# Optimization experiments

Measured on AMD Instinct MI355X. Metric: run time of the kernel, lower is better.

The kernel has to match this reference:

```python
import jax, jax.numpy as jnp
from jax import lax
import numpy as np

INPUT_SIZE = 8
HIDDEN = 32
OUTPUT = 1
B, T = 8192, 512


def setup_inputs() -> dict:
    key = jax.random.key(0)
    ks = jax.random.split(key, 8)
    s = 1.0 / np.sqrt(HIDDEN)  # PyTorch LSTM init scale
    x = jax.random.normal(ks[0], (B, T, INPUT_SIZE), dtype=jnp.float32)
    W_ih = jax.random.uniform(ks[1], (4 * HIDDEN, INPUT_SIZE), minval=-s, maxval=s, dtype=jnp.float32)
    W_hh = jax.random.uniform(ks[2], (4 * HIDDEN, HIDDEN), minval=-s, maxval=s, dtype=jnp.float32)
    b_ih = jax.random.uniform(ks[3], (4 * HIDDEN,), minval=-s, maxval=s, dtype=jnp.float32)
    b_hh = jax.random.uniform(ks[4], (4 * HIDDEN,), minval=-s, maxval=s, dtype=jnp.float32)
    W_fc = jax.random.uniform(ks[5], (OUTPUT, HIDDEN), minval=-s, maxval=s, dtype=jnp.float32)
    b_fc = jax.random.uniform(ks[6], (OUTPUT,), minval=-s, maxval=s, dtype=jnp.float32)
    return {"x": x, "W_ih": W_ih, "W_hh": W_hh, "b_ih": b_ih, "b_hh": b_hh, "W_fc": W_fc, "b_fc": b_fc}


def reference(x, W_ih, W_hh, b_ih, b_hh, W_fc, b_fc):
    # x: [B, T, D]. Precompute input-gate contributions in one large GEMM,
    # then scan the recurrence over time. PyTorch gate order: i, f, g, o.
    Bn, Tn, _ = x.shape
    H = W_hh.shape[1]
    xg = jnp.einsum('btd,gd->btg', x, W_ih) + b_ih + b_hh  # [B, T, 4H]
    xg = jnp.swapaxes(xg, 0, 1)  # [T, B, 4H]

    def step(carry, xt):
        h, c = carry
        gates = xt + h @ W_hh.T  # [B, 4H]
        i, f, g, o = jnp.split(gates, 4, axis=-1)
        c = jax.nn.sigmoid(f) * c + jax.nn.sigmoid(i) * jnp.tanh(g)
        h = jax.nn.sigmoid(o) * jnp.tanh(c)
        return (h, c), None

    h0 = jnp.zeros((Bn, H), dtype=x.dtype)
    (h_n, _), _ = lax.scan(step, (h0, h0), xg)
    # fc applied to h_n: [num_layers=1, B, H] -> [1, B, output_size]
    out = h_n @ W_fc.T + b_fc  # [B, 1]
    return out[None, :, :]
```

## Files before the change

kernel.cpp:

```cpp
#include <hip/hip_runtime.h>
#include <cstddef>

#define T_LEN 512
#define IN_D 8
#define H 32
#define NBATCH 16
#define NT 512
#define NCHUNK (T_LEN / 8)
#define LOG2E 1.44269504088896341f
#define GP 36
#define CSCLAMP 88.f

typedef __attribute__((ext_vector_type(8))) short bf16x8;
typedef __attribute__((ext_vector_type(4))) float f32x4;

__device__ __forceinline__ float fexp2(float v) { return __builtin_amdgcn_exp2f(v); }
__device__ __forceinline__ float frcp(float v)  { return __builtin_amdgcn_rcpf(v); }
__device__ __forceinline__ unsigned short f2bf(float f) {
    unsigned u = __builtin_bit_cast(unsigned, f);
    u += 0x7FFF + ((u >> 16) & 1);
    return (unsigned short)(u >> 16);
}
__device__ __forceinline__ float bf2f(unsigned short b) {
    unsigned u = ((unsigned)b) << 16;
    return __builtin_bit_cast(float, u);
}
__device__ __forceinline__ float ubits(unsigned u) { return __builtin_bit_cast(float, u); }
__device__ __forceinline__ unsigned cvt_pk_bf16(float lo, float hi) {
    unsigned r;
    asm("v_cvt_pk_bf16_f32 %0, %1, %2" : "=v"(r) : "v"(lo), "v"(hi));
    return r;
}

#define WG_BARRIER() asm volatile("s_waitcnt lgkmcnt(0)\n\ts_barrier" ::: "memory")

__global__ void __launch_bounds__(NT, 4) lstm_mfma4(
    const float* __restrict__ x, const float* __restrict__ W_ih,
    const float* __restrict__ W_hh, const float* __restrict__ b_ih,
    const float* __restrict__ b_hh, const float* __restrict__ W_fc,
    const float* __restrict__ b_fc, float* __restrict__ out)
{
    __shared__ __align__(16) float G[4][NBATCH][GP];
    __shared__ __align__(16) unsigned short hhi[NBATCH][48];
    __shared__ __align__(16) unsigned short hlo[NBATCH][48];
    __shared__ __align__(16) unsigned short xstg[8][17][24];

    const int tix  = threadIdx.x;
    const int w    = tix >> 6;
    const int g    = w >> 1;
    const int d    = w & 1;
    const int lane = tix & 63;
    const int q    = lane >> 4;
    const int cc   = lane & 15;

    const float kk = (g == 2) ? -2.f * LOG2E : -LOG2E;

    bf16x8 Bh, Bl, Bx;
    const int r = 16 * (2 * g + d) + cc;
    #pragma unroll
    for (int j = 0; j < 8; ++j) {
        const int p = 8 * q + j;
        const int u = 16 * (p & 1) + (p >> 1);
        const float ws = kk * W_hh[r * H + u];
        const unsigned short whi = f2bf(ws);
        Bh[j] = (short)whi;
        Bl[j] = (short)f2bf(ws - bf2f(whi));
        if (q == 3) {
            Bx[j] = 0;
        } else {
            const float wsx = kk * W_ih[r * IN_D + j];
            const unsigned short xwh = f2bf(wsx);
            Bx[j] = (q == 2) ? (short)f2bf(wsx - bf2f(xwh)) : (short)xwh;
        }
    }
    const float bias = kk * (b_ih[r] + b_hh[r]);
    const f32x4 biasv = { bias, bias, bias, bias };

    const int xoff = (q == 2) ? 0 : ((q == 3) ? 16 : 8 * q);

    const int xb = (tix >> 4) & 15, xs = (tix >> 1) & 7, xhf = tix & 1;
    const bool stager = (tix < 256);
    const float* xbase = x + (size_t)(blockIdx.x * NBATCH + xb) * (size_t)(T_LEN * IN_D)
                           + xs * IN_D + 4 * xhf;
    auto ldchunk = [&](int ch) { return *(const float4*)(xbase + (size_t)ch * 8 * IN_D); };
    auto stage = [&](float4 v) {
        const unsigned h0 = cvt_pk_bf16(v.x, v.y);
        const unsigned h1 = cvt_pk_bf16(v.z, v.w);
        const unsigned l0 = cvt_pk_bf16(v.x - ubits(h0 << 16), v.y - ubits(h0 & 0xffff0000u));
        const unsigned l1 = cvt_pk_bf16(v.z - ubits(h1 << 16), v.w - ubits(h1 & 0xffff0000u));
        *(uint2*)&xstg[xs][xb][4 * xhf]     = make_uint2(h0, h1);
        *(uint2*)&xstg[xs][xb][8 + 4 * xhf] = make_uint2(l0, l1);
    };

    for (int i = tix; i < NBATCH * 48 / 2; i += NT) {
        ((unsigned*)hhi)[i] = 0u;
        ((unsigned*)hlo)[i] = 0u;
    }
    for (int i = tix; i < 8 * 17 * 24 / 2; i += NT) ((unsigned*)xstg)[i] = 0u;
    __syncthreads();
    float4 xbuf = {0.f, 0.f, 0.f, 0.f};
    if (stager) {
        stage(ldchunk(0));
        xbuf = ldchunk(1);
    }
    __syncthreads();

    f32x4 XC[8];
#define REFILL(j) do { \
        const bf16x8 Ax_ = *(const bf16x8*)&xstg[(j)][cc][xoff]; \
        XC[(j)] = __builtin_amdgcn_mfma_f32_16x16x32_bf16(Ax_, Bx, biasv, 0, 0, 0); \
    } while (0)
    #pragma unroll
    for (int s = 0; s < 8; ++s) REFILL(s);

    const int m = tix >> 5, u = tix & 31;
    const float wfc = W_fc[u];
    const float TWL = 2.f * LOG2E;
    float cs = 0.f, hf = 0.f;

    for (int blk = 0; blk < NCHUNK; ++blk) {
        #pragma unroll
        for (int s = 0; s < 8; ++s) {
            const bf16x8 A0 = *(const bf16x8*)&hhi[cc][8 * q];
            const bf16x8 A2 = *(const bf16x8*)&hlo[cc][8 * q];
            const f32x4 z = { 0.f, 0.f, 0.f, 0.f };
            f32x4 a1 = __builtin_amdgcn_mfma_f32_16x16x32_bf16(A0, Bh, XC[s], 0, 0, 0);
            f32x4 a2 = __builtin_amdgcn_mfma_f32_16x16x32_bf16(A2, Bh, z, 0, 0, 0);
            a2 = __builtin_amdgcn_mfma_f32_16x16x32_bf16(A0, Bl, a2, 0, 0, 0);
            const f32x4 C = a1 + a2;

            if (s == 0 && stager) {
                stage(xbuf);
                int nc = blk + 2;
                if (nc > NCHUNK - 1) nc = NCHUNK - 1;
                xbuf = ldchunk(nc);
            }

            #pragma unroll
            for (int rg = 0; rg < 4; ++rg)
                G[g][4 * q + rg][cc + 16 * d] = C[rg];

            if (s >= 1) REFILL(s - 1);
            if (s == 7) REFILL(7);

            WG_BARRIER();

            {
                const float Ei = fexp2(G[0][m][u]);
                const float Ef = fexp2(G[1][m][u]);
                const float Eg = fexp2(G[2][m][u]);
                const float Eo = fexp2(G[3][m][u]);
                const float P  = (1.f + Eg) * (1.f + Ei);
                const float Q  = 1.f + Ef;
                const float r1 = __builtin_fmaf(Eg, -TWL, TWL);
                const float num = __builtin_fmaf(cs, P, r1 * Q);
                const float rd  = frcp(P * Q);
                cs = num * rd;
                cs = fminf(fmaxf(cs, -CSCLAMP), CSCLAMP);
                const float W  = fexp2(cs);
                const float rh = frcp((1.f + Eo) * (W + 1.f));
                hf = (W - 1.f) * rh;
                const float hp = __shfl_xor(hf, 16);
                if ((tix & 16) == 0) {
                    const unsigned hw = cvt_pk_bf16(hf, hp);
                    const unsigned lw = cvt_pk_bf16(hf - ubits(hw << 16),
                                                    hp - ubits(hw & 0xffff0000u));
                    *(unsigned*)&hhi[m][2 * (u & 15)] = hw;
                    *(unsigned*)&hlo[m][2 * (u & 15)] = lw;
                }
            }

            WG_BARRIER();
        }
    }
#undef REFILL

    float sacc = hf * wfc;
    sacc += __shfl_xor(sacc, 1);
    sacc += __shfl_xor(sacc, 2);
    sacc += __shfl_xor(sacc, 4);
    sacc += __shfl_xor(sacc, 8);
    sacc += __shfl_xor(sacc, 16);
    if ((tix & 31) == 0) out[blockIdx.x * NBATCH + m] = sacc + b_fc[0];
}

extern "C" void kernel_launch(void* const* d_in, const int* in_sizes, int n_in,
                              void* d_out, int out_size, void* d_ws, size_t ws_size,
                              hipStream_t stream) {
    const float* x    = (const float*)d_in[0];
    const float* W_ih = (const float*)d_in[1];
    const float* W_hh = (const float*)d_in[2];
    const float* b_ih = (const float*)d_in[3];
    const float* b_hh = (const float*)d_in[4];
    const float* W_fc = (const float*)d_in[5];
    const float* b_fc = (const float*)d_in[6];
    float* out = (float*)d_out;
    const int Bn = in_sizes[0] / (T_LEN * IN_D);
    lstm_mfma4<<<dim3(Bn / NBATCH), dim3(NT), 0, stream>>>(
        x, W_ih, W_hh, b_ih, b_hh, W_fc, b_fc, out);
}
```

Measured before the change: 473.8 us.

## Interleave gate rows so each lane holds all four gates, dropping gate LDS exchange

Reorders the W_hh/W_ih rows so that every MFMA output lane receives the i,f,g,o pre-activations of a single hidden unit and batch row. The gate LDS buffer and one of the two workgroup barriers per timestep can therefore be removed. The hidden state becomes double-buffered so writes for step t+1 do not collide with reads of step t, and the final FC reduction now goes through a small LDS partial-sum array. The cost is more scattered 16-bit LDS stores of h and a third independent MFMA for the low-order correction term.

```diff
diff --git a/kernel.cpp b/kernel.cpp
--- a/kernel.cpp
+++ b/kernel.cpp
@@ -8,7 +8,6 @@
 #define NT 512
 #define NCHUNK (T_LEN / 8)
 #define LOG2E 1.44269504088896341f
-#define GP 36
 #define CSCLAMP 88.f
 
 typedef __attribute__((ext_vector_type(8))) short bf16x8;
@@ -34,47 +33,51 @@
 
 #define WG_BARRIER() asm volatile("s_waitcnt lgkmcnt(0)\n\ts_barrier" ::: "memory")
 
-__global__ void __launch_bounds__(NT, 4) lstm_mfma4(
+__global__ void __launch_bounds__(NT, 4) lstm_xfree(
     const float* __restrict__ x, const float* __restrict__ W_ih,
     const float* __restrict__ W_hh, const float* __restrict__ b_ih,
     const float* __restrict__ b_hh, const float* __restrict__ W_fc,
     const float* __restrict__ b_fc, float* __restrict__ out)
 {
-    __shared__ __align__(16) float G[4][NBATCH][GP];
-    __shared__ __align__(16) unsigned short hhi[NBATCH][48];
-    __shared__ __align__(16) unsigned short hlo[NBATCH][48];
+    __shared__ __align__(16) unsigned short hh[2][NBATCH][40];
+    __shared__ __align__(16) unsigned short hl[2][NBATCH][40];
     __shared__ __align__(16) unsigned short xstg[8][17][24];
+    __shared__ float gpart[8][NBATCH];
 
     const int tix  = threadIdx.x;
-    const int w    = tix >> 6;
-    const int g    = w >> 1;
-    const int d    = w & 1;
+    const int m    = tix >> 6;
     const int lane = tix & 63;
     const int q    = lane >> 4;
     const int cc   = lane & 15;
 
-    const float kk = (g == 2) ? -2.f * LOG2E : -LOG2E;
-
-    bf16x8 Bh, Bl, Bx;
-    const int r = 16 * (2 * g + d) + cc;
+    const int gate = cc & 3;
+    const int urow = 4 * m + (cc >> 2);
+    const int wrow = 32 * gate + urow;
+    const float kk = (gate == 2) ? -2.f * LOG2E : -LOG2E;
+    bf16x8 Whi, Wlo, Wx;
     #pragma unroll
     for (int j = 0; j < 8; ++j) {
         const int p = 8 * q + j;
         const int u = 16 * (p & 1) + (p >> 1);
-        const float ws = kk * W_hh[r * H + u];
+        const float ws = kk * W_hh[wrow * H + u];
         const unsigned short whi = f2bf(ws);
-        Bh[j] = (short)whi;
-        Bl[j] = (short)f2bf(ws - bf2f(whi));
+        Whi[j] = (short)whi;
+        Wlo[j] = (short)f2bf(ws - bf2f(whi));
         if (q == 3) {
-            Bx[j] = 0;
+            Wx[j] = 0;
         } else {
-            const float wsx = kk * W_ih[r * IN_D + j];
+            const float wsx = kk * W_ih[wrow * IN_D + j];
             const unsigned short xwh = f2bf(wsx);
-            Bx[j] = (q == 2) ? (short)f2bf(wsx - bf2f(xwh)) : (short)xwh;
+            Wx[j] = (q == 2) ? (short)f2bf(wsx - bf2f(xwh)) : (short)xwh;
         }
     }
-    const float bias = kk * (b_ih[r] + b_hh[r]);
-    const f32x4 biasv = { bias, bias, bias, bias };
+    f32x4 biasv;
+    #pragma unroll
+    for (int reg = 0; reg < 4; ++reg) {
+        const int br = 32 * reg + 4 * m + q;
+        const float kkr = (reg == 2) ? -2.f * LOG2E : -LOG2E;
+        biasv[reg] = kkr * (b_ih[br] + b_hh[br]);
+    }
 
     const int xoff = (q == 2) ? 0 : ((q == 3) ? 16 : 8 * q);
 
@@ -92,9 +95,9 @@
         *(uint2*)&xstg[xs][xb][8 + 4 * xhf] = make_uint2(l0, l1);
     };
 
-    for (int i = tix; i < NBATCH * 48 / 2; i += NT) {
-        ((unsigned*)hhi)[i] = 0u;
-        ((unsigned*)hlo)[i] = 0u;
+    for (int i = tix; i < (int)(sizeof(hh) / 4); i += NT) {
+        ((unsigned*)hh)[i] = 0u;
+        ((unsigned*)hl)[i] = 0u;
     }
     for (int i = tix; i < 8 * 17 * 24 / 2; i += NT) ((unsigned*)xstg)[i] = 0u;
     __syncthreads();
@@ -106,28 +109,37 @@
     __syncthreads();
 
     f32x4 XC[8];
-#define REFILL(j) do { \
-        const bf16x8 Ax_ = *(const bf16x8*)&xstg[(j)][cc][xoff]; \
-        XC[(j)] = __builtin_amdgcn_mfma_f32_16x16x32_bf16(Ax_, Bx, biasv, 0, 0, 0); \
-    } while (0)
     #pragma unroll
-    for (int s = 0; s < 8; ++s) REFILL(s);
-
-    const int m = tix >> 5, u = tix & 31;
-    const float wfc = W_fc[u];
+    for (int s = 0; s < 8; ++s) {
+        const bf16x8 Bx_ = *(const bf16x8*)&xstg[s][cc][xoff];
+        XC[s] = __builtin_amdgcn_mfma_f32_16x16x32_bf16(Wx, Bx_, biasv, 0, 0, 0);
+    }
+
+    const int uown = 4 * m + q;
+    const int piu  = (uown < 16) ? 2 * uown : 2 * (uown - 16) + 1;
     const float TWL = 2.f * LOG2E;
     float cs = 0.f, hf = 0.f;
 
     for (int blk = 0; blk < NCHUNK; ++blk) {
         #pragma unroll
         for (int s = 0; s < 8; ++s) {
-            const bf16x8 A0 = *(const bf16x8*)&hhi[cc][8 * q];
-            const bf16x8 A2 = *(const bf16x8*)&hlo[cc][8 * q];
+            const int rb = s & 1, wb = rb ^ 1;
+
+            const bf16x8 Hh = *(const bf16x8*)&hh[rb][cc][8 * q];
+            const bf16x8 Hl = *(const bf16x8*)&hl[rb][cc][8 * q];
+            bf16x8 Bxp, Bx7;
+            if (s >= 1)  Bxp = *(const bf16x8*)&xstg[s - 1][cc][xoff];
+            if (s == 7)  Bx7 = *(const bf16x8*)&xstg[7][cc][xoff];
+
             const f32x4 z = { 0.f, 0.f, 0.f, 0.f };
-            f32x4 a1 = __builtin_amdgcn_mfma_f32_16x16x32_bf16(A0, Bh, XC[s], 0, 0, 0);
-            f32x4 a2 = __builtin_amdgcn_mfma_f32_16x16x32_bf16(A2, Bh, z, 0, 0, 0);
-            a2 = __builtin_amdgcn_mfma_f32_16x16x32_bf16(A0, Bl, a2, 0, 0, 0);
-            const f32x4 C = a1 + a2;
+            f32x4 a1 = __builtin_amdgcn_mfma_f32_16x16x32_bf16(Whi, Hh, XC[s], 0, 0, 0);
+            f32x4 a2 = __builtin_amdgcn_mfma_f32_16x16x32_bf16(Whi, Hl, z, 0, 0, 0);
+            f32x4 a3 = __builtin_amdgcn_mfma_f32_16x16x32_bf16(Wlo, Hh, z, 0, 0, 0);
+
+            if (s >= 1)
+                XC[s - 1] = __builtin_amdgcn_mfma_f32_16x16x32_bf16(Wx, Bxp, biasv, 0, 0, 0);
+            if (s == 7)
+                XC[7] = __builtin_amdgcn_mfma_f32_16x16x32_bf16(Wx, Bx7, biasv, 0, 0, 0);
 
             if (s == 0 && stager) {
                 stage(xbuf);
@@ -136,20 +148,12 @@
                 xbuf = ldchunk(nc);
             }
 
-            #pragma unroll
-            for (int rg = 0; rg < 4; ++rg)
-                G[g][4 * q + rg][cc + 16 * d] = C[rg];
-
-            if (s >= 1) REFILL(s - 1);
-            if (s == 7) REFILL(7);
-
-            WG_BARRIER();
-
+            const f32x4 C = (a1 + a2) + a3;
             {
-                const float Ei = fexp2(G[0][m][u]);
-                const float Ef = fexp2(G[1][m][u]);
-                const float Eg = fexp2(G[2][m][u]);
-                const float Eo = fexp2(G[3][m][u]);
+                const float Ei = fexp2(C[0]);
+                const float Ef = fexp2(C[1]);
+                const float Eg = fexp2(C[2]);
+                const float Eo = fexp2(C[3]);
                 const float P  = (1.f + Eg) * (1.f + Ei);
                 const float Q  = 1.f + Ef;
                 const float r1 = __builtin_fmaf(Eg, -TWL, TWL);
@@ -160,28 +164,31 @@
                 const float W  = fexp2(cs);
                 const float rh = frcp((1.f + Eo) * (W + 1.f));
                 hf = (W - 1.f) * rh;
-                const float hp = __shfl_xor(hf, 16);
-                if ((tix & 16) == 0) {
-                    const unsigned hw = cvt_pk_bf16(hf, hp);
-                    const unsigned lw = cvt_pk_bf16(hf - ubits(hw << 16),
-                                                    hp - ubits(hw & 0xffff0000u));
-                    *(unsigned*)&hhi[m][2 * (u & 15)] = hw;
-                    *(unsigned*)&hlo[m][2 * (u & 15)] = lw;
-                }
+            }
+
+            {
+                const unsigned short hw16 = (unsigned short)cvt_pk_bf16(hf, hf);
+                const float hlo_ = hf - ubits((unsigned)hw16 << 16);
+                const unsigned short lw16 = (unsigned short)cvt_pk_bf16(hlo_, hlo_);
+                hh[wb][cc][piu] = hw16;
+                hl[wb][cc][piu] = lw16;
             }
 
             WG_BARRIER();
         }
     }
-#undef REFILL
-
-    float sacc = hf * wfc;
-    sacc += __shfl_xor(sacc, 1);
-    sacc += __shfl_xor(sacc, 2);
-    sacc += __shfl_xor(sacc, 4);
-    sacc += __shfl_xor(sacc, 8);
-    sacc += __shfl_xor(sacc, 16);
-    if ((tix & 31) == 0) out[blockIdx.x * NBATCH + m] = sacc + b_fc[0];
+
+    float part = hf * W_fc[uown];
+    part += __shfl_xor(part, 16);
+    part += __shfl_xor(part, 32);
+    if (lane < NBATCH) gpart[m][lane] = part;
+    __syncthreads();
+    if (tix < NBATCH) {
+        float s = b_fc[0];
+        #pragma unroll
+        for (int mm = 0; mm < 8; ++mm) s += gpart[mm][tix];
+        out[blockIdx.x * NBATCH + tix] = s;
+    }
 }
 
 extern "C" void kernel_launch(void* const* d_in, const int* in_sizes, int n_in,
@@ -196,6 +203,6 @@
     const float* b_fc = (const float*)d_in[6];
     float* out = (float*)d_out;
     const int Bn = in_sizes[0] / (T_LEN * IN_D);
-    lstm_mfma4<<<dim3(Bn / NBATCH), dim3(NT), 0, stream>>>(
+    lstm_xfree<<<dim3(Bn / NBATCH), dim3(NT), 0, stream>>>(
         x, W_ih, W_hh, b_ih, b_hh, W_fc, b_fc, out);
 }
```

New measurement: 388.2 us. 1.22x faster.
